# Kernel tuning notes

Hardware: AMD Instinct MI355X
Metric: run time of the kernel (lower is better)

Reference implementation:

```python
import jax, jax.numpy as jnp
import numpy as np

D_IN = 32
D_MODEL = 128
B, T = 512, 512
INPUT_DIM = 2 * D_IN  # concat_mask=True, d_u=0


def setup_inputs() -> dict:
    key = jax.random.key(0)
    ks = jax.random.split(key, 8)
    scale = 0.05
    return {
        "x": jax.random.normal(ks[0], (B, T, D_IN), dtype=jnp.float32),
        "W_ih": jax.random.normal(ks[1], (3 * D_MODEL, INPUT_DIM), dtype=jnp.float32) * scale,
        "W_hh": jax.random.normal(ks[2], (3 * D_MODEL, D_MODEL), dtype=jnp.float32) * scale,
        "b_ih": jax.random.normal(ks[3], (3 * D_MODEL,), dtype=jnp.float32) * scale,
        "b_hh": jax.random.normal(ks[4], (3 * D_MODEL,), dtype=jnp.float32) * scale,
        "W_out": jax.random.normal(ks[5], (D_IN, D_MODEL), dtype=jnp.float32) * scale,
        "b_out": jax.random.normal(ks[6], (D_IN,), dtype=jnp.float32) * scale,
        "mask": jax.random.randint(ks[7], (B, T, D_IN), 0, 2, dtype=jnp.int32),
    }


def reference(x, W_ih, W_hh, b_ih, b_hh, W_out, b_out, mask):
    m_bool = mask.astype(bool)                      # [B,T,d_in]
    m_f = mask.astype(x.dtype)
    x = jnp.where(m_bool, x, jnp.zeros_like(x))     # zero-fill missing

    h0 = jnp.zeros((x.shape[0], D_MODEL), dtype=x.dtype)   # state_init='zero'
    x_hat0 = h0 @ W_out.T + b_out                   # readout of initial state

    def gru_cell(x_t, h):
        gx = x_t @ W_ih.T + b_ih                    # [B, 3*d_model]
        gh = h @ W_hh.T + b_hh
        xr, xz, xn = jnp.split(gx, 3, axis=-1)
        hr, hz, hn = jnp.split(gh, 3, axis=-1)
        r = jax.nn.sigmoid(xr + hr)
        z = jax.nn.sigmoid(xz + hz)
        n = jnp.tanh(xn + r * hn)
        return (1.0 - z) * n + z * h

    def step(carry, inp):
        h, x_hat = carry
        x_s, mb_s, mf_s = inp                       # [B,d_in] each
        x_p = jnp.where(mb_s, x_s, x_hat)           # fill blanks with prediction
        x_t = jnp.concatenate([x_p, mf_s], axis=-1) # concat_mask=True
        h_new = gru_cell(x_t, h)
        x_hat_new = h_new @ W_out.T + b_out
        return (h_new, x_hat_new), x_hat_new

    # scan over steps 0..T-2 (time-major)
    xs = jnp.swapaxes(x[:, :-1], 0, 1)              # [T-1, B, d_in]
    mbs = jnp.swapaxes(m_bool[:, :-1], 0, 1)
    mfs = jnp.swapaxes(m_f[:, :-1], 0, 1)
    _, preds = jax.lax.scan(step, (h0, x_hat0), (xs, mbs, mfs))  # [T-1, B, d_in]

    out = jnp.concatenate([x_hat0[None], preds], axis=0)         # [T, B, d_in]
    return jnp.swapaxes(out, 0, 1)                                # [B, T, d_in]
```

## Files before the change

### kernel.cpp

```cpp
#include <hip/hip_runtime.h>
#include <hip/hip_bf16.h>

#define D_IN 32
#define TT 512
#define GB 16
#define NBLK 32
#define MAGIC 0x51F7C0DEu

typedef __attribute__((ext_vector_type(8))) short bf16x8;
typedef __attribute__((ext_vector_type(4))) float f32x4;
typedef __attribute__((ext_vector_type(4))) int   i32x4;

__device__ inline short bf16_of(float f) {
    union { float f; unsigned u; } v; v.f = f;
    unsigned r = v.u + 0x7FFFu + ((v.u >> 16) & 1u);
    return (short)(r >> 16);
}
__device__ inline unsigned cvt_pk_bf16(float lo, float hi) {
    unsigned r;
    asm("v_cvt_pk_bf16_f32 %0, %1, %2" : "=v"(r) : "v"(lo), "v"(hi));
    return r;
}
__device__ inline bf16x8 load8_bf16(const float* __restrict__ p) {
    bf16x8 r;
#pragma unroll
    for (int e = 0; e < 8; ++e) r[e] = bf16_of(p[e]);
    return r;
}
__device__ inline bf16x8 load44_bf16(const float* __restrict__ p, int qq) {
    bf16x8 r;
#pragma unroll
    for (int e = 0; e < 4; ++e) {
        r[e]     = bf16_of(p[qq * 4 + e]);
        r[4 + e] = bf16_of(p[16 + qq * 4 + e]);
    }
    return r;
}
__device__ inline f32x4 splat4(float v) { return (f32x4){v, v, v, v}; }

__device__ inline float sigmoid_fast(float x) {
    return __builtin_amdgcn_rcpf(1.0f + __expf(-x));
}
__device__ inline float tanh_fast(float x) {
    return 1.0f - 2.0f * __builtin_amdgcn_rcpf(__expf(2.0f * x) + 1.0f);
}
__device__ inline void lds_barrier() {
    asm volatile("s_waitcnt lgkmcnt(0)\n\ts_barrier" ::: "memory");
}

__global__ __launch_bounds__(512, 2)
void rnn_imputer(const float* __restrict__ x,
                 const float* __restrict__ W_ih,
                 const float* __restrict__ W_hh,
                 const float* __restrict__ b_ih,
                 const float* __restrict__ b_hh,
                 const float* __restrict__ W_out,
                 const float* __restrict__ b_out,
                 const int*   __restrict__ mask,
                 float* __restrict__ out,
                 unsigned*    flags,
                 int          use_spin) {
    if (blockIdx.x >= NBLK) {
        if (!use_spin || threadIdx.x >= 64) return;
        const unsigned long long t0 = __builtin_amdgcn_s_memrealtime();
        float a0 = 1.0f + threadIdx.x * 1e-6f, a1 = a0 + 0.1f, a2 = a0 + 0.2f,
              a3 = a0 + 0.3f, a4 = a0 + 0.4f, a5 = a0 + 0.5f, a6 = a0 + 0.6f,
              a7 = a0 + 0.7f;
        for (;;) {
            unsigned acc = 0;
#pragma unroll
            for (int j = 0; j < NBLK; ++j)
                acc |= (__hip_atomic_load(&flags[j], __ATOMIC_RELAXED,
                                          __HIP_MEMORY_SCOPE_AGENT) ^ MAGIC);
            if (acc == 0) break;
            if (__builtin_amdgcn_s_memrealtime() - t0 > 200000ull) break;
            for (int i = 0; i < 32; ++i) {
                a0 = __builtin_fmaf(a0, 1.0000001f, 1e-8f);
                a1 = __builtin_fmaf(a1, 1.0000001f, 1e-8f);
                a2 = __builtin_fmaf(a2, 1.0000001f, 1e-8f);
                a3 = __builtin_fmaf(a3, 1.0000001f, 1e-8f);
                a4 = __builtin_fmaf(a4, 1.0000001f, 1e-8f);
                a5 = __builtin_fmaf(a5, 1.0000001f, 1e-8f);
                a6 = __builtin_fmaf(a6, 1.0000001f, 1e-8f);
                a7 = __builtin_fmaf(a7, 1.0000001f, 1e-8f);
            }
            __builtin_amdgcn_s_sleep(24);
        }
        const float s = a0 + a1 + a2 + a3 + a4 + a5 + a6 + a7;
        if (s == 1.2345e30f) ((float*)flags)[NBLK + 1] = s;
        return;
    }

    __shared__ __align__(16) float xch[16][GB][36];
    __shared__ __align__(16) int   mch[16][GB][36];
    __shared__ __align__(16) short hbuf[2][GB][136];

    const int tid  = threadIdx.x;
    const int wv   = tid >> 6;
    const int lane = tid & 63;
    const int q    = lane >> 4;
    const int c    = lane & 15;
    const int bb   = blockIdx.x * GB;
    const int brow = bb + c;
    const int i_col = wv * 16 + c;

    bf16x8 Br[6], Bz[6], Bxn[2], Bhn[4];
    Br[0]  = load44_bf16(W_ih + (size_t)i_col * 64, q);
    Br[1]  = load44_bf16(W_ih + (size_t)i_col * 64 + 32, q);
    Bz[0]  = load44_bf16(W_ih + (size_t)(128 + i_col) * 64, q);
    Bz[1]  = load44_bf16(W_ih + (size_t)(128 + i_col) * 64 + 32, q);
    Bxn[0] = load44_bf16(W_ih + (size_t)(256 + i_col) * 64, q);
    Bxn[1] = load44_bf16(W_ih + (size_t)(256 + i_col) * 64 + 32, q);
#pragma unroll
    for (int kt = 2; kt < 6; ++kt) {
        const int k = (kt - 2) * 32 + q * 8;
        Br[kt] = load8_bf16(W_hh + (size_t)i_col * 128 + k);
        Bz[kt] = load8_bf16(W_hh + (size_t)(128 + i_col) * 128 + k);
    }
#pragma unroll
    for (int kt = 0; kt < 4; ++kt)
        Bhn[kt] = load8_bf16(W_hh + (size_t)(256 + i_col) * 128 + kt * 32 + q * 8);

    bf16x8 Ao[2][4];
#pragma unroll
    for (int ta = 0; ta < 2; ++ta)
#pragma unroll
        for (int kt = 0; kt < 4; ++kt)
            Ao[ta][kt] = load8_bf16(W_out + (size_t)(ta * 16 + c) * 128 + kt * 32 + q * 8);

    f32x4 bo_v[2];
#pragma unroll
    for (int ta = 0; ta < 2; ++ta)
        bo_v[ta] = *(const f32x4*)&b_out[ta * 16 + q * 4];

    const float bR  = b_ih[i_col]       + b_hh[i_col];
    const float bZ  = b_ih[128 + i_col] + b_hh[128 + i_col];
    const float bXN = b_ih[256 + i_col];
    const float bHN = b_hh[256 + i_col];

    float h_reg[4] = {0.f, 0.f, 0.f, 0.f};

    bf16x8 A0, A1;
    {
        const size_t o = (size_t)brow * TT * D_IN;
        const f32x4 xa = *(const f32x4*)&x[o + q * 4];
        const f32x4 xb = *(const f32x4*)&x[o + 16 + q * 4];
        const i32x4 ma = *(const i32x4*)&mask[o + q * 4];
        const i32x4 mb = *(const i32x4*)&mask[o + 16 + q * 4];
        union { bf16x8 v; unsigned d[4]; } a0, a1;
#pragma unroll
        for (int j = 0; j < 4; ++j) {
            const float fa = ma[j] ? xa[j] : b_out[q * 4 + j];
            const float fb = mb[j] ? xb[j] : b_out[16 + q * 4 + j];
            ((short*)&a0.v)[j]     = bf16_of(fa);
            ((short*)&a0.v)[4 + j] = bf16_of(fb);
            ((short*)&a1.v)[j]     = ma[j] ? (short)0x3F80 : (short)0;
            ((short*)&a1.v)[4 + j] = mb[j] ? (short)0x3F80 : (short)0;
        }
        A0 = a0.v; A1 = a1.v;
    }
#pragma unroll
    for (int ta = 0; ta < 2; ++ta)
        if (wv == ta)
            *(f32x4*)&out[(size_t)brow * TT * D_IN + ta * 16 + q * 4] = bo_v[ta];

#pragma unroll
    for (int rnd = 0; rnd < 4; ++rnd) {
        const int ts  = 1 + rnd * 4 + (tid >> 7);
        const int row = (tid >> 3) & 15;
        const int c4  = (tid & 7) * 4;
        const size_t o = ((size_t)(bb + row) * TT + ts) * D_IN + c4;
        *(f32x4*)&xch[ts & 15][row][c4] = *(const f32x4*)&x[o];
        *(i32x4*)&mch[ts & 15][row][c4] = *(const i32x4*)&mask[o];
    }

    f32x4 Ra = __builtin_amdgcn_mfma_f32_16x16x32_bf16(A1, Br[1],  splat4(bR), 0, 0, 0);
    f32x4 Za = __builtin_amdgcn_mfma_f32_16x16x32_bf16(A1, Bz[1],  splat4(bZ), 0, 0, 0);
    f32x4 XN = __builtin_amdgcn_mfma_f32_16x16x32_bf16(A1, Bxn[1], splat4(bXN), 0, 0, 0);
    f32x4 Rb = splat4(0.f), Zb = splat4(0.f);
    f32x4 HNa = splat4(bHN), HNb = splat4(0.f);

    f32x4 sgx[2] = {splat4(0.f), splat4(0.f)};
    i32x4 sgm[2] = {(i32x4){0,0,0,0}, (i32x4){0,0,0,0}};

    __syncthreads();

    for (int t = 0; t < TT - 1; ++t) {
        Rb = __builtin_amdgcn_mfma_f32_16x16x32_bf16(A0, Br[0],  Rb, 0, 0, 0);
        Zb = __builtin_amdgcn_mfma_f32_16x16x32_bf16(A0, Bz[0],  Zb, 0, 0, 0);
        XN = __builtin_amdgcn_mfma_f32_16x16x32_bf16(A0, Bxn[0], XN, 0, 0, 0);

        const int sl = (t + 1) & 15;
        const f32x4 pfx0 = *(const f32x4*)&xch[sl][c][q * 4];
        const f32x4 pfx1 = *(const f32x4*)&xch[sl][c][16 + q * 4];
        const i32x4 pfm0 = *(const i32x4*)&mch[sl][c][q * 4];
        const i32x4 pfm1 = *(const i32x4*)&mch[sl][c][16 + q * 4];

        if ((t & 7) == 0 && t) {
#pragma unroll
            for (int rnd = 0; rnd < 2; ++rnd) {
                const int tsu = t + 8 + rnd * 4 + (tid >> 7);
                const int row = (tid >> 3) & 15;
                const int c4  = (tid & 7) * 4;
                *(f32x4*)&xch[tsu & 15][row][c4] = sgx[rnd];
                *(i32x4*)&mch[tsu & 15][row][c4] = sgm[rnd];
            }
        }
        if ((t & 7) == 7) {
#pragma unroll
            for (int rnd = 0; rnd < 2; ++rnd) {
                const int tsu = t + 9 + rnd * 4 + (tid >> 7);
                const int ts  = tsu <= TT - 1 ? tsu : TT - 1;
                const int row = (tid >> 3) & 15;
                const int c4  = (tid & 7) * 4;
                const size_t o = ((size_t)(bb + row) * TT + ts) * D_IN + c4;
                sgx[rnd] = *(const f32x4*)&x[o];
                sgm[rnd] = *(const i32x4*)&mask[o];
            }
        }

        const int pb = (t + 1) & 1;
#pragma unroll
        for (int r = 0; r < 4; ++r) {
            const float rr = sigmoid_fast(Ra[r] + Rb[r]);
            const float zz = sigmoid_fast(Za[r] + Zb[r]);
            const float nn = tanh_fast(XN[r] + rr * (HNa[r] + HNb[r]));
            const float h  = nn + zz * (h_reg[r] - nn);
            h_reg[r] = h;
            hbuf[pb][q * 4 + r][i_col] = bf16_of(h);
        }

        lds_barrier();

        bf16x8 Ah[4];
#pragma unroll
        for (int kt = 0; kt < 4; ++kt)
            Ah[kt] = *(const bf16x8*)&hbuf[pb][c][kt * 32 + q * 8];

        f32x4 aO0a = __builtin_amdgcn_mfma_f32_16x16x32_bf16(Ao[0][0], Ah[0], bo_v[0], 0, 0, 0);
        f32x4 aO1a = __builtin_amdgcn_mfma_f32_16x16x32_bf16(Ao[1][0], Ah[0], bo_v[1], 0, 0, 0);
        f32x4 aO0b = __builtin_amdgcn_mfma_f32_16x16x32_bf16(Ao[0][2], Ah[2], splat4(0.f), 0, 0, 0);
        f32x4 aO1b = __builtin_amdgcn_mfma_f32_16x16x32_bf16(Ao[1][2], Ah[2], splat4(0.f), 0, 0, 0);
        aO0a = __builtin_amdgcn_mfma_f32_16x16x32_bf16(Ao[0][1], Ah[1], aO0a, 0, 0, 0);
        aO1a = __builtin_amdgcn_mfma_f32_16x16x32_bf16(Ao[1][1], Ah[1], aO1a, 0, 0, 0);
        aO0b = __builtin_amdgcn_mfma_f32_16x16x32_bf16(Ao[0][3], Ah[3], aO0b, 0, 0, 0);
        aO1b = __builtin_amdgcn_mfma_f32_16x16x32_bf16(Ao[1][3], Ah[3], aO1b, 0, 0, 0);

        Ra  = __builtin_amdgcn_mfma_f32_16x16x32_bf16(Ah[0], Br[2], splat4(bR), 0, 0, 0);
        Za  = __builtin_amdgcn_mfma_f32_16x16x32_bf16(Ah[0], Bz[2], splat4(bZ), 0, 0, 0);
        HNa = __builtin_amdgcn_mfma_f32_16x16x32_bf16(Ah[0], Bhn[0], splat4(bHN), 0, 0, 0);
        Rb  = __builtin_amdgcn_mfma_f32_16x16x32_bf16(Ah[2], Br[4], splat4(0.f), 0, 0, 0);
        Zb  = __builtin_amdgcn_mfma_f32_16x16x32_bf16(Ah[2], Bz[4], splat4(0.f), 0, 0, 0);
        Ra  = __builtin_amdgcn_mfma_f32_16x16x32_bf16(Ah[1], Br[3], Ra, 0, 0, 0);
        Za  = __builtin_amdgcn_mfma_f32_16x16x32_bf16(Ah[1], Bz[3], Za, 0, 0, 0);
        HNa = __builtin_amdgcn_mfma_f32_16x16x32_bf16(Ah[1], Bhn[1], HNa, 0, 0, 0);
        Rb  = __builtin_amdgcn_mfma_f32_16x16x32_bf16(Ah[3], Br[5], Rb, 0, 0, 0);
        Zb  = __builtin_amdgcn_mfma_f32_16x16x32_bf16(Ah[3], Bz[5], Zb, 0, 0, 0);
        HNb = __builtin_amdgcn_mfma_f32_16x16x32_bf16(Ah[2], Bhn[2], splat4(0.f), 0, 0, 0);
        HNb = __builtin_amdgcn_mfma_f32_16x16x32_bf16(Ah[3], Bhn[3], HNb, 0, 0, 0);

        {
            union { bf16x8 v; unsigned d[4]; } a1;
            a1.d[0] = (pfm0[0] ? 0x3F80u : 0u) | ((pfm0[1] ? 0x3F80u : 0u) << 16);
            a1.d[1] = (pfm0[2] ? 0x3F80u : 0u) | ((pfm0[3] ? 0x3F80u : 0u) << 16);
            a1.d[2] = (pfm1[0] ? 0x3F80u : 0u) | ((pfm1[1] ? 0x3F80u : 0u) << 16);
            a1.d[3] = (pfm1[2] ? 0x3F80u : 0u) | ((pfm1[3] ? 0x3F80u : 0u) << 16);
            A1 = a1.v;
        }
        Ra = __builtin_amdgcn_mfma_f32_16x16x32_bf16(A1, Br[1],  Ra, 0, 0, 0);
        Za = __builtin_amdgcn_mfma_f32_16x16x32_bf16(A1, Bz[1],  Za, 0, 0, 0);
        XN = __builtin_amdgcn_mfma_f32_16x16x32_bf16(A1, Bxn[1], splat4(bXN), 0, 0, 0);

        {
            f32x4 xh0, xh1;
#pragma unroll
            for (int r = 0; r < 4; ++r) {
                xh0[r] = aO0a[r] + aO0b[r];
                xh1[r] = aO1a[r] + aO1b[r];
            }
            if (wv == 0)
                *(f32x4*)&out[((size_t)brow * TT + (t + 1)) * D_IN + q * 4] = xh0;
            if (wv == 1)
                *(f32x4*)&out[((size_t)brow * TT + (t + 1)) * D_IN + 16 + q * 4] = xh1;

            const float v00 = pfm0[0] ? pfx0[0] : xh0[0];
            const float v01 = pfm0[1] ? pfx0[1] : xh0[1];
            const float v02 = pfm0[2] ? pfx0[2] : xh0[2];
            const float v03 = pfm0[3] ? pfx0[3] : xh0[3];
            const float v10 = pfm1[0] ? pfx1[0] : xh1[0];
            const float v11 = pfm1[1] ? pfx1[1] : xh1[1];
            const float v12 = pfm1[2] ? pfx1[2] : xh1[2];
            const float v13 = pfm1[3] ? pfx1[3] : xh1[3];
            union { bf16x8 v; unsigned d[4]; } a0;
            a0.d[0] = cvt_pk_bf16(v00, v01);
            a0.d[1] = cvt_pk_bf16(v02, v03);
            a0.d[2] = cvt_pk_bf16(v10, v11);
            a0.d[3] = cvt_pk_bf16(v12, v13);
            A0 = a0.v;
        }
    }

    if (use_spin && tid == 0)
        __hip_atomic_store(&flags[blockIdx.x], MAGIC, __ATOMIC_RELAXED,
                           __HIP_MEMORY_SCOPE_AGENT);
}

extern "C" void kernel_launch(void* const* d_in, const int* in_sizes, int n_in,
                              void* d_out, int out_size, void* d_ws, size_t ws_size,
                              hipStream_t stream) {
    const float* x     = (const float*)d_in[0];
    const float* W_ih  = (const float*)d_in[1];
    const float* W_hh  = (const float*)d_in[2];
    const float* b_ih  = (const float*)d_in[3];
    const float* b_hh  = (const float*)d_in[4];
    const float* W_out = (const float*)d_in[5];
    const float* b_out = (const float*)d_in[6];
    const int*   mask  = (const int*)d_in[7];
    float* out = (float*)d_out;

    const int use_spin = (d_ws != nullptr && ws_size >= 256) ? 1 : 0;
    const int grid = use_spin ? 256 : NBLK;

    rnn_imputer<<<dim3(grid), dim3(512), 0, stream>>>(
        x, W_ih, W_hh, b_ih, b_hh, W_out, b_out, mask, out,
        (unsigned*)d_ws, use_spin);
}
```

Before: 666.1 us.

## Split readout MFMAs across two waves and share input operands via LDS

Previously every wave computed both halves of the output readout (8 MFMAs) redundantly. Now waves 0 and 1 each compute one 16-column half (4 MFMAs), write their output slice, and publish the blended input and mask bf16 fragments to LDS. All waves then read A0/A1 back after an extra barrier. The input-side MFMAs for the mask half are moved to the top of the next step. This trims redundant matrix work on the serial recurrence path but adds a second workgroup barrier per timestep.

```diff
diff --git a/kernel.cpp b/kernel.cpp
--- a/kernel.cpp
+++ b/kernel.cpp
@@ -10,6 +10,7 @@
 typedef __attribute__((ext_vector_type(8))) short bf16x8;
 typedef __attribute__((ext_vector_type(4))) float f32x4;
 typedef __attribute__((ext_vector_type(4))) int   i32x4;
+typedef __attribute__((ext_vector_type(2))) unsigned u32x2;
 
 __device__ inline short bf16_of(float f) {
     union { float f; unsigned u; } v; v.f = f;
@@ -94,6 +95,8 @@
     __shared__ __align__(16) float xch[16][GB][36];
     __shared__ __align__(16) int   mch[16][GB][36];
     __shared__ __align__(16) short hbuf[2][GB][136];
+    __shared__ __align__(16) unsigned a0sh[4][16][4];
+    __shared__ __align__(16) unsigned a1sh[4][16][4];
 
     const int tid  = threadIdx.x;
     const int wv   = tid >> 6;
@@ -174,9 +177,7 @@
         *(i32x4*)&mch[ts & 15][row][c4] = *(const i32x4*)&mask[o];
     }
 
-    f32x4 Ra = __builtin_amdgcn_mfma_f32_16x16x32_bf16(A1, Br[1],  splat4(bR), 0, 0, 0);
-    f32x4 Za = __builtin_amdgcn_mfma_f32_16x16x32_bf16(A1, Bz[1],  splat4(bZ), 0, 0, 0);
-    f32x4 XN = __builtin_amdgcn_mfma_f32_16x16x32_bf16(A1, Bxn[1], splat4(bXN), 0, 0, 0);
+    f32x4 Ra = splat4(bR), Za = splat4(bZ);
     f32x4 Rb = splat4(0.f), Zb = splat4(0.f);
     f32x4 HNa = splat4(bHN), HNb = splat4(0.f);
 
@@ -188,13 +189,18 @@
     for (int t = 0; t < TT - 1; ++t) {
         Rb = __builtin_amdgcn_mfma_f32_16x16x32_bf16(A0, Br[0],  Rb, 0, 0, 0);
         Zb = __builtin_amdgcn_mfma_f32_16x16x32_bf16(A0, Bz[0],  Zb, 0, 0, 0);
-        XN = __builtin_amdgcn_mfma_f32_16x16x32_bf16(A0, Bxn[0], XN, 0, 0, 0);
+        f32x4 XNb = __builtin_amdgcn_mfma_f32_16x16x32_bf16(A0, Bxn[0], splat4(0.f), 0, 0, 0);
+        Ra = __builtin_amdgcn_mfma_f32_16x16x32_bf16(A1, Br[1],  Ra, 0, 0, 0);
+        Za = __builtin_amdgcn_mfma_f32_16x16x32_bf16(A1, Bz[1],  Za, 0, 0, 0);
+        f32x4 XNa = __builtin_amdgcn_mfma_f32_16x16x32_bf16(A1, Bxn[1], splat4(bXN), 0, 0, 0);
 
         const int sl = (t + 1) & 15;
-        const f32x4 pfx0 = *(const f32x4*)&xch[sl][c][q * 4];
-        const f32x4 pfx1 = *(const f32x4*)&xch[sl][c][16 + q * 4];
-        const i32x4 pfm0 = *(const i32x4*)&mch[sl][c][q * 4];
-        const i32x4 pfm1 = *(const i32x4*)&mch[sl][c][16 + q * 4];
+        f32x4 pfx = splat4(0.f);
+        i32x4 pfm = (i32x4){0, 0, 0, 0};
+        if (wv < 2) {
+            pfx = *(const f32x4*)&xch[sl][c][wv * 16 + q * 4];
+            pfm = *(const i32x4*)&mch[sl][c][wv * 16 + q * 4];
+        }
 
         if ((t & 7) == 0 && t) {
 #pragma unroll
@@ -220,14 +226,23 @@
         }
 
         const int pb = (t + 1) & 1;
+        float hn[4];
 #pragma unroll
         for (int r = 0; r < 4; ++r) {
             const float rr = sigmoid_fast(Ra[r] + Rb[r]);
             const float zz = sigmoid_fast(Za[r] + Zb[r]);
-            const float nn = tanh_fast(XN[r] + rr * (HNa[r] + HNb[r]));
+            const float nn = tanh_fast(XNa[r] + XNb[r] + rr * (HNa[r] + HNb[r]));
             const float h  = nn + zz * (h_reg[r] - nn);
             h_reg[r] = h;
-            hbuf[pb][q * 4 + r][i_col] = bf16_of(h);
+            hn[r] = h;
+        }
+        {
+            const unsigned pk0 = cvt_pk_bf16(hn[0], hn[1]);
+            const unsigned pk1 = cvt_pk_bf16(hn[2], hn[3]);
+            hbuf[pb][q * 4 + 0][i_col] = (short)(pk0 & 0xFFFFu);
+            hbuf[pb][q * 4 + 1][i_col] = (short)(pk0 >> 16);
+            hbuf[pb][q * 4 + 2][i_col] = (short)(pk1 & 0xFFFFu);
+            hbuf[pb][q * 4 + 3][i_col] = (short)(pk1 >> 16);
         }
 
         lds_barrier();
@@ -237,14 +252,13 @@
         for (int kt = 0; kt < 4; ++kt)
             Ah[kt] = *(const bf16x8*)&hbuf[pb][c][kt * 32 + q * 8];
 
-        f32x4 aO0a = __builtin_amdgcn_mfma_f32_16x16x32_bf16(Ao[0][0], Ah[0], bo_v[0], 0, 0, 0);
-        f32x4 aO1a = __builtin_amdgcn_mfma_f32_16x16x32_bf16(Ao[1][0], Ah[0], bo_v[1], 0, 0, 0);
-        f32x4 aO0b = __builtin_amdgcn_mfma_f32_16x16x32_bf16(Ao[0][2], Ah[2], splat4(0.f), 0, 0, 0);
-        f32x4 aO1b = __builtin_amdgcn_mfma_f32_16x16x32_bf16(Ao[1][2], Ah[2], splat4(0.f), 0, 0, 0);
-        aO0a = __builtin_amdgcn_mfma_f32_16x16x32_bf16(Ao[0][1], Ah[1], aO0a, 0, 0, 0);
-        aO1a = __builtin_amdgcn_mfma_f32_16x16x32_bf16(Ao[1][1], Ah[1], aO1a, 0, 0, 0);
-        aO0b = __builtin_amdgcn_mfma_f32_16x16x32_bf16(Ao[0][3], Ah[3], aO0b, 0, 0, 0);
-        aO1b = __builtin_amdgcn_mfma_f32_16x16x32_bf16(Ao[1][3], Ah[3], aO1b, 0, 0, 0);
+        f32x4 roA = splat4(0.f), roB = splat4(0.f);
+        if (wv < 2) {
+            roA = __builtin_amdgcn_mfma_f32_16x16x32_bf16(Ao[wv][0], Ah[0], bo_v[wv], 0, 0, 0);
+            roB = __builtin_amdgcn_mfma_f32_16x16x32_bf16(Ao[wv][2], Ah[2], splat4(0.f), 0, 0, 0);
+            roA = __builtin_amdgcn_mfma_f32_16x16x32_bf16(Ao[wv][1], Ah[1], roA, 0, 0, 0);
+            roB = __builtin_amdgcn_mfma_f32_16x16x32_bf16(Ao[wv][3], Ah[3], roB, 0, 0, 0);
+        }
 
         Ra  = __builtin_amdgcn_mfma_f32_16x16x32_bf16(Ah[0], Br[2], splat4(bR), 0, 0, 0);
         Za  = __builtin_amdgcn_mfma_f32_16x16x32_bf16(Ah[0], Bz[2], splat4(bZ), 0, 0, 0);
@@ -259,45 +273,30 @@
         HNb = __builtin_amdgcn_mfma_f32_16x16x32_bf16(Ah[2], Bhn[2], splat4(0.f), 0, 0, 0);
         HNb = __builtin_amdgcn_mfma_f32_16x16x32_bf16(Ah[3], Bhn[3], HNb, 0, 0, 0);
 
-        {
-            union { bf16x8 v; unsigned d[4]; } a1;
-            a1.d[0] = (pfm0[0] ? 0x3F80u : 0u) | ((pfm0[1] ? 0x3F80u : 0u) << 16);
-            a1.d[1] = (pfm0[2] ? 0x3F80u : 0u) | ((pfm0[3] ? 0x3F80u : 0u) << 16);
-            a1.d[2] = (pfm1[0] ? 0x3F80u : 0u) | ((pfm1[1] ? 0x3F80u : 0u) << 16);
-            a1.d[3] = (pfm1[2] ? 0x3F80u : 0u) | ((pfm1[3] ? 0x3F80u : 0u) << 16);
-            A1 = a1.v;
-        }
-        Ra = __builtin_amdgcn_mfma_f32_16x16x32_bf16(A1, Br[1],  Ra, 0, 0, 0);
-        Za = __builtin_amdgcn_mfma_f32_16x16x32_bf16(A1, Bz[1],  Za, 0, 0, 0);
-        XN = __builtin_amdgcn_mfma_f32_16x16x32_bf16(A1, Bxn[1], splat4(bXN), 0, 0, 0);
-
-        {
-            f32x4 xh0, xh1;
-#pragma unroll
-            for (int r = 0; r < 4; ++r) {
-                xh0[r] = aO0a[r] + aO0b[r];
-                xh1[r] = aO1a[r] + aO1b[r];
-            }
-            if (wv == 0)
-                *(f32x4*)&out[((size_t)brow * TT + (t + 1)) * D_IN + q * 4] = xh0;
-            if (wv == 1)
-                *(f32x4*)&out[((size_t)brow * TT + (t + 1)) * D_IN + 16 + q * 4] = xh1;
-
-            const float v00 = pfm0[0] ? pfx0[0] : xh0[0];
-            const float v01 = pfm0[1] ? pfx0[1] : xh0[1];
-            const float v02 = pfm0[2] ? pfx0[2] : xh0[2];
-            const float v03 = pfm0[3] ? pfx0[3] : xh0[3];
-            const float v10 = pfm1[0] ? pfx1[0] : xh1[0];
-            const float v11 = pfm1[1] ? pfx1[1] : xh1[1];
-            const float v12 = pfm1[2] ? pfx1[2] : xh1[2];
-            const float v13 = pfm1[3] ? pfx1[3] : xh1[3];
-            union { bf16x8 v; unsigned d[4]; } a0;
-            a0.d[0] = cvt_pk_bf16(v00, v01);
-            a0.d[1] = cvt_pk_bf16(v02, v03);
-            a0.d[2] = cvt_pk_bf16(v10, v11);
-            a0.d[3] = cvt_pk_bf16(v12, v13);
-            A0 = a0.v;
-        }
+        if (wv < 2) {
+            f32x4 xh;
+#pragma unroll
+            for (int r = 0; r < 4; ++r) xh[r] = roA[r] + roB[r];
+            *(f32x4*)&out[((size_t)brow * TT + (t + 1)) * D_IN + wv * 16 + q * 4] = xh;
+
+            const float v0 = pfm[0] ? pfx[0] : xh[0];
+            const float v1 = pfm[1] ? pfx[1] : xh[1];
+            const float v2 = pfm[2] ? pfx[2] : xh[2];
+            const float v3 = pfm[3] ? pfx[3] : xh[3];
+            u32x2 pa;
+            pa[0] = cvt_pk_bf16(v0, v1);
+            pa[1] = cvt_pk_bf16(v2, v3);
+            *(u32x2*)&a0sh[q][c][wv * 2] = pa;
+            u32x2 pm;
+            pm[0] = (pfm[0] ? 0x3F80u : 0u) | ((pfm[1] ? 0x3F80u : 0u) << 16);
+            pm[1] = (pfm[2] ? 0x3F80u : 0u) | ((pfm[3] ? 0x3F80u : 0u) << 16);
+            *(u32x2*)&a1sh[q][c][wv * 2] = pm;
+        }
+
+        lds_barrier();
+
+        A0 = *(const bf16x8*)&a0sh[q][c][0];
+        A1 = *(const bf16x8*)&a1sh[q][c][0];
     }
 
     if (use_spin && tid == 0)
```

After: 719.3 us. 8.0% more time.
